# Kernel optimization log

Measured on AMD Instinct MI355X. Metric: run time of the kernel, lower is better.

Reference implementation:

```python
import jax, jax.numpy as jnp
import numpy as np

CUTOFF = 2.0
LOG2 = float(np.log(2.0))

def ssp(x):
    # shifted softplus: softplus(x) - log(2)
    return jax.nn.softplus(x) - LOG2

def setup_inputs() -> dict:
    key = jax.random.key(0)
    ks = jax.random.split(key, 12)
    N, E, H, F, G = 10000, 320000, 256, 256, 50
    x = jax.random.normal(ks[0], (N, H), dtype=jnp.float32)
    edge_index = jax.random.randint(ks[1], (2, E), 0, N, dtype=jnp.int64)
    edge_weight = jax.random.normal(ks[2], (E, 3), dtype=jnp.float32)
    edge_attr = jax.random.normal(ks[3], (E, G), dtype=jnp.float32)
    s = lambda fan_in: 1.0 / np.sqrt(fan_in)
    mlp_w1 = jax.random.uniform(ks[4], (G, F), jnp.float32, -s(G), s(G))
    mlp_b1 = jax.random.uniform(ks[5], (F,), jnp.float32, -s(G), s(G))
    mlp_w2 = jax.random.uniform(ks[6], (F, F), jnp.float32, -s(F), s(F))
    mlp_b2 = jax.random.uniform(ks[7], (F,), jnp.float32, -s(F), s(F))
    lin1_w = jax.random.uniform(ks[8], (H, F), jnp.float32, -s(H), s(H))
    lin2_w = jax.random.uniform(ks[9], (F, H), jnp.float32, -s(F), s(F))
    lin2_b = jax.random.uniform(ks[10], (H,), jnp.float32, -s(F), s(F))
    return {"x": x, "edge_index": edge_index, "edge_weight": edge_weight,
            "edge_attr": edge_attr, "mlp_w1": mlp_w1, "mlp_b1": mlp_b1,
            "mlp_w2": mlp_w2, "mlp_b2": mlp_b2, "lin1_w": lin1_w,
            "lin2_w": lin2_w, "lin2_b": lin2_b}

def reference(x, edge_index, edge_weight, edge_attr,
              mlp_w1, mlp_b1, mlp_w2, mlp_b2, lin1_w, lin2_w, lin2_b):
    N = x.shape[0]
    # cutoff envelope on edge distances
    distances = jnp.linalg.norm(edge_weight, axis=1)                 # [E]
    C = 0.5 * (jnp.cos(distances * jnp.pi / CUTOFF) + 1.0)
    C = C * (distances <= CUTOFF)                                    # [E]
    # edge filter MLP
    W = ssp(edge_attr @ mlp_w1 + mlp_b1) @ mlp_w2 + mlp_b2           # [E, F]
    W = W * C[:, None]
    i, j = edge_index[0], edge_index[1]
    messages = W * (x[j] @ lin1_w)                                   # [E, F]
    agg = jax.ops.segment_sum(messages, i, num_segments=N)           # [N, F]
    h = ssp(agg @ lin2_w + lin2_b)                                   # [N, H]
    return x + h
```

## Files before the change

### kernel.cpp

```cpp
#include <hip/hip_runtime.h>
#include <hip/hip_bf16.h>
#include <stdint.h>

#define HF 256
#define GG 50

typedef __attribute__((ext_vector_type(8))) short bf16x8;
typedef __attribute__((ext_vector_type(4))) short bf16x4;
typedef __attribute__((ext_vector_type(4))) float f32x4;

__device__ __forceinline__ uint32_t f2bf2u(float a, float b){
    __hip_bfloat162 h = __float22bfloat162_rn(make_float2(a, b));
    union { __hip_bfloat162 h; uint32_t u; } v; v.h = h; return v.u;
}
__device__ __forceinline__ short f2bf(float x){
    union { float f; uint32_t u; } v; v.f = x;
    uint32_t r = (v.u + 0x7FFFu + ((v.u >> 16) & 1u)) >> 16;
    return (short)(uint16_t)r;
}
__device__ __forceinline__ float bf2f(short s){
    union { uint32_t u; float f; } v; v.u = ((uint32_t)(uint16_t)s) << 16;
    return v.f;
}
__device__ __forceinline__ float ssp_f(float x){
    return fmaxf(x, 0.f) + __logf(1.f + __expf(-fabsf(x))) - 0.69314718055994531f;
}

__device__ __forceinline__ void pack_natural(const float* __restrict__ B,
                                             short* __restrict__ Bp,
                                             int idx, int KT, int kmax)
{
    int lane = idx & 63;
    int kt   = (idx >> 6) & (KT - 1);
    int ntg  = idx >> (6 + (KT == 2 ? 1 : 3));
    int col  = ntg * 16 + (lane & 15);
    int k0   = kt * 32 + (lane >> 4) * 8;
    uint32_t u[4];
#pragma unroll
    for (int jj = 0; jj < 4; ++jj) {
        int ka = k0 + 2*jj, kb = k0 + 2*jj + 1;
        float a = (ka < kmax) ? B[(size_t)ka * HF + col] : 0.f;
        float b = (kb < kmax) ? B[(size_t)kb * HF + col] : 0.f;
        u[jj] = f2bf2u(a, b);
    }
    *(uint4*)&Bp[(size_t)idx * 8] = *(uint4*)u;
}

__global__ __launch_bounds__(256)
void prep_kernel(const float* __restrict__ w1, const float* __restrict__ w2,
                 const float* __restrict__ lin1, const float* __restrict__ lin2,
                 short* __restrict__ w1p, short* __restrict__ w2p,
                 short* __restrict__ lin1p, short* __restrict__ lin2p,
                 const float* __restrict__ x, short* __restrict__ x_bf, int nx8,
                 const int* __restrict__ eidx, int* __restrict__ cnt, int E, int gConv)
{
    int b = blockIdx.x, tid = threadIdx.x;
    if (b < 8) {
        pack_natural(w1, w1p, b * 256 + tid, 2, GG);
    } else if (b < 40) {
        int idx = (b - 8) * 256 + tid;
        int lane = idx & 63;
        int kt   = (idx >> 6) & 7;
        int ntg  = idx >> 9;
        int col  = ntg * 16 + (lane & 15);
        int s0   = kt * 32 + (lane >> 4) * 8;
        uint32_t u[4];
#pragma unroll
        for (int jj = 0; jj < 4; ++jj) {
            int sa = s0 + 2*jj, sb = sa + 1;
            int fa = (sa >> 6) * 64 + (sa & 3) * 16 + ((sa & 63) >> 2);
            int fb = (sb >> 6) * 64 + (sb & 3) * 16 + ((sb & 63) >> 2);
            u[jj] = f2bf2u(w2[(size_t)fa * HF + col], w2[(size_t)fb * HF + col]);
        }
        *(uint4*)&w2p[(size_t)idx * 8] = *(uint4*)u;
    } else if (b < 72) {
        pack_natural(lin1, lin1p, (b - 40) * 256 + tid, 8, HF);
    } else if (b < 104) {
        pack_natural(lin2, lin2p, (b - 72) * 256 + tid, 8, HF);
    } else if (b < 104 + gConv) {
        int idx = (b - 104) * 256 + tid;
        if (idx < nx8) {
            const float* xp = x + (size_t)idx * 8;
            float4 p0 = *(const float4*)(xp);
            float4 p1 = *(const float4*)(xp + 4);
            uint32_t u[4] = { f2bf2u(p0.x, p0.y), f2bf2u(p0.z, p0.w),
                              f2bf2u(p1.x, p1.y), f2bf2u(p1.z, p1.w) };
            *(uint4*)&x_bf[(size_t)idx * 8] = *(uint4*)u;
        }
    } else {
        int e = (b - 104 - gConv) * 256 + tid;
        if (e < E) atomicAdd(&cnt[eidx[e]], 1);
    }
}

__global__ __launch_bounds__(256)
void scan_kernel(const int* __restrict__ cnt, int* __restrict__ row,
                 int* __restrict__ cursor, int N, int E)
{
    __shared__ int part[256];
    const int t = threadIdx.x;
    const int CH = (N + 255) / 256;
    int lo = t * CH;
    int hi = min(lo + CH, N);
    int s = 0;
    for (int n = lo; n < hi; ++n) s += cnt[n];
    part[t] = s;
    __syncthreads();
    for (int off = 1; off < 256; off <<= 1) {
        int v = (t >= off) ? part[t - off] : 0;
        __syncthreads();
        part[t] += v;
        __syncthreads();
    }
    int acc = part[t] - s;
    for (int n = lo; n < hi; ++n) {
        row[n] = acc; cursor[n] = acc;
        acc += cnt[n];
    }
    if (t == 255) row[N] = E;
}

__global__ __launch_bounds__(256)
void mid_kernel(const int* __restrict__ eidx, int* __restrict__ cursor,
                int* __restrict__ perm, int E, int gScatter,
                const short* __restrict__ x_bf, const short* __restrict__ lin1p,
                short* __restrict__ y_p, int N)
{
    const int tid = threadIdx.x;
    if ((int)blockIdx.x < gScatter) {
        int e = blockIdx.x * 256 + tid;
        if (e < E) {
            int pos = atomicAdd(&cursor[eidx[e]], 1);
            perm[pos] = e;
        }
        return;
    }
    const int blk  = blockIdx.x - gScatter;
    const int lane = tid & 63;
    const int w    = tid >> 6;
    const int l15  = lane & 15;
    const int quad = lane >> 4;
    const int row0 = blk * 64;

    f32x4 acc[4][4];
#pragma unroll
    for (int mt = 0; mt < 4; ++mt)
#pragma unroll
        for (int nt = 0; nt < 4; ++nt)
            acc[mt][nt] = (f32x4){0.f, 0.f, 0.f, 0.f};

#pragma unroll 2
    for (int kt = 0; kt < 8; ++kt) {
        bf16x8 af[4];
#pragma unroll
        for (int mt = 0; mt < 4; ++mt) {
            int r = row0 + mt * 16 + l15;
            int rl = (r < N) ? r : 0;
            af[mt] = *(const bf16x8*)&x_bf[(size_t)rl * HF + kt * 32 + quad * 8];
        }
#pragma unroll
        for (int nt = 0; nt < 4; ++nt) {
            bf16x8 bfr = *(const bf16x8*)&lin1p[(size_t)(((w * 4 + nt) * 8 + kt) * 64 + lane) * 8];
#pragma unroll
            for (int mt = 0; mt < 4; ++mt)
                acc[mt][nt] = __builtin_amdgcn_mfma_f32_16x16x32_bf16(af[mt], bfr, acc[mt][nt], 0, 0, 0);
        }
    }
#pragma unroll
    for (int mt = 0; mt < 4; ++mt) {
#pragma unroll
        for (int r = 0; r < 4; ++r) {
            int row = row0 + mt * 16 + quad * 4 + r;
            if (row < N) {
                uint2 u = make_uint2(f2bf2u(acc[mt][0][r], acc[mt][1][r]),
                                     f2bf2u(acc[mt][2][r], acc[mt][3][r]));
                *(uint2*)&y_p[(size_t)row * HF + w * 64 + l15 * 4] = u;
            }
        }
    }
}

__global__ __launch_bounds__(256)
void node2_kernel(const float* __restrict__ agg, const short* __restrict__ lin2p,
                  const float* __restrict__ bias, const float* __restrict__ x,
                  float* __restrict__ out, int N)
{
    const int tid  = threadIdx.x;
    const int lane = tid & 63;
    const int w    = tid >> 6;
    const int l15  = lane & 15;
    const int quad = lane >> 4;
    const int row0 = blockIdx.x * 64;

    f32x4 acc[4][4];
#pragma unroll
    for (int mt = 0; mt < 4; ++mt)
#pragma unroll
        for (int nt = 0; nt < 4; ++nt)
            acc[mt][nt] = (f32x4){0.f, 0.f, 0.f, 0.f};

#pragma unroll 2
    for (int kt = 0; kt < 8; ++kt) {
        bf16x8 af[4];
#pragma unroll
        for (int mt = 0; mt < 4; ++mt) {
            int r = row0 + mt * 16 + l15;
            int rl = (r < N) ? r : 0;
            const float* ap = agg + (size_t)rl * HF + kt * 32 + quad * 8;
            float4 p0 = *(const float4*)(ap);
            float4 p1 = *(const float4*)(ap + 4);
            union { uint32_t u[4]; bf16x8 v; } c;
            c.u[0] = f2bf2u(p0.x, p0.y); c.u[1] = f2bf2u(p0.z, p0.w);
            c.u[2] = f2bf2u(p1.x, p1.y); c.u[3] = f2bf2u(p1.z, p1.w);
            af[mt] = c.v;
        }
#pragma unroll
        for (int nt = 0; nt < 4; ++nt) {
            bf16x8 bfr = *(const bf16x8*)&lin2p[(size_t)(((w * 4 + nt) * 8 + kt) * 64 + lane) * 8];
#pragma unroll
            for (int mt = 0; mt < 4; ++mt)
                acc[mt][nt] = __builtin_amdgcn_mfma_f32_16x16x32_bf16(af[mt], bfr, acc[mt][nt], 0, 0, 0);
        }
    }
    float bs[4];
#pragma unroll
    for (int nt = 0; nt < 4; ++nt) bs[nt] = bias[w * 64 + nt * 16 + l15];
#pragma unroll
    for (int mt = 0; mt < 4; ++mt) {
#pragma unroll
        for (int r = 0; r < 4; ++r) {
            int row = row0 + mt * 16 + quad * 4 + r;
            if (row < N) {
#pragma unroll
                for (int nt = 0; nt < 4; ++nt) {
                    int f = w * 64 + nt * 16 + l15;
                    float v = ssp_f(acc[mt][nt][r] + bs[nt]) + x[(size_t)row * HF + f];
                    out[(size_t)row * HF + f] = v;
                }
            }
        }
    }
}

__global__ __launch_bounds__(256, 3)
void edge_mfma(const float* __restrict__ ea, const int* __restrict__ eidx,
               const float* __restrict__ ew,
               const short* __restrict__ w1p, const float* __restrict__ b1,
               const short* __restrict__ w2p, const float* __restrict__ b2,
               const short* __restrict__ y_p, const int* __restrict__ perm,
               const int* __restrict__ rowp,
               float* __restrict__ agg, int E)
{
    __shared__ short smem[21504];
    short* ea_b = smem;
    short* hid  = smem + 4608;
    short* msgT = smem;
    __shared__ int s_e[64], s_i[64], s_j[64];
    __shared__ float s_c[64];
    __shared__ unsigned long long s_bmask;

    const int tid  = threadIdx.x;
    const int lane = tid & 63;
    const int w    = tid >> 6;
    const int l15  = lane & 15;
    const int quad = lane >> 4;
    const int e0   = blockIdx.x * 64;

    if (tid < 64) {
        int p = e0 + tid;
        int e = 0, iv = -1, jv = 0;
        float c = 0.f;
        if (p < E) {
            e  = perm[p];
            iv = eidx[e];
            jv = eidx[E + e];
            float d0 = ew[e*3+0], d1 = ew[e*3+1], d2 = ew[e*3+2];
            float d = sqrtf(d0*d0 + d1*d1 + d2*d2);
            c = (d <= 2.0f) ? 0.5f * (__cosf(d * 1.57079632679489662f) + 1.0f) : 0.f;
        }
        s_e[tid] = e; s_i[tid] = iv; s_j[tid] = jv; s_c[tid] = c;
        int ivn = __shfl_down(iv, 1);
        bool flag = (tid == 63) || (iv != ivn);
        unsigned long long m = __ballot(flag);
        if (tid == 0) s_bmask = m;
    }
    __syncthreads();

    for (int idx = tid; idx < 64 * 25; idx += 256) {
        int e = idx / 25, p = idx - e * 25;
        const float* sp = ea + (size_t)s_e[e] * GG + p * 2;
        float2 v = *(const float2*)sp;
        *(uint32_t*)&ea_b[e * 72 + p * 2] = f2bf2u(v.x, v.y);
    }
    for (int idx = tid; idx < 64 * 7; idx += 256) {
        int e = idx / 7, q = idx - e * 7;
        *(uint32_t*)&ea_b[e * 72 + 50 + q * 2] = 0u;
    }
    __syncthreads();

    f32x4 acc1[4][4];
#pragma unroll
    for (int mt = 0; mt < 4; ++mt)
#pragma unroll
        for (int nt = 0; nt < 4; ++nt)
            acc1[mt][nt] = (f32x4){0.f, 0.f, 0.f, 0.f};

#pragma unroll
    for (int kt = 0; kt < 2; ++kt) {
        bf16x8 af[4];
#pragma unroll
        for (int mt = 0; mt < 4; ++mt)
            af[mt] = *(bf16x8*)&ea_b[(mt * 16 + l15) * 72 + kt * 32 + quad * 8];
#pragma unroll
        for (int nt = 0; nt < 4; ++nt) {
            bf16x8 bfr = *(const bf16x8*)&w1p[(size_t)(((w * 4 + nt) * 2 + kt) * 64 + lane) * 8];
#pragma unroll
            for (int mt = 0; mt < 4; ++mt)
                acc1[mt][nt] = __builtin_amdgcn_mfma_f32_16x16x32_bf16(af[mt], bfr, acc1[mt][nt], 0, 0, 0);
        }
    }

    float bias1[4];
#pragma unroll
    for (int nt = 0; nt < 4; ++nt) bias1[nt] = b1[w * 64 + nt * 16 + l15];
#pragma unroll
    for (int mt = 0; mt < 4; ++mt) {
#pragma unroll
        for (int r = 0; r < 4; ++r) {
            int e = mt * 16 + quad * 4 + r;
            float v0 = ssp_f(acc1[mt][0][r] + bias1[0]);
            float v1 = ssp_f(acc1[mt][1][r] + bias1[1]);
            float v2 = ssp_f(acc1[mt][2][r] + bias1[2]);
            float v3 = ssp_f(acc1[mt][3][r] + bias1[3]);
            uint2 u = make_uint2(f2bf2u(v0, v1), f2bf2u(v2, v3));
            *(uint2*)&hid[e * 264 + w * 64 + l15 * 4] = u;
        }
    }
    __syncthreads();

    bf16x4 yv[4][4];
#pragma unroll
    for (int mt = 0; mt < 4; ++mt)
#pragma unroll
        for (int r = 0; r < 4; ++r) {
            int e = mt * 16 + quad * 4 + r;
            yv[mt][r] = *(const bf16x4*)&y_p[(size_t)s_j[e] * HF + w * 64 + l15 * 4];
        }

    f32x4 acc2[4][4];
#pragma unroll
    for (int mt = 0; mt < 4; ++mt)
#pragma unroll
        for (int nt = 0; nt < 4; ++nt)
            acc2[mt][nt] = (f32x4){0.f, 0.f, 0.f, 0.f};

#pragma unroll 2
    for (int kt = 0; kt < 8; ++kt) {
        bf16x8 af[4];
#pragma unroll
        for (int mt = 0; mt < 4; ++mt)
            af[mt] = *(bf16x8*)&hid[(mt * 16 + l15) * 264 + kt * 32 + quad * 8];
#pragma unroll
        for (int nt = 0; nt < 4; ++nt) {
            bf16x8 bfr = *(const bf16x8*)&w2p[(size_t)(((w * 4 + nt) * 8 + kt) * 64 + lane) * 8];
#pragma unroll
            for (int mt = 0; mt < 4; ++mt)
                acc2[mt][nt] = __builtin_amdgcn_mfma_f32_16x16x32_bf16(af[mt], bfr, acc2[mt][nt], 0, 0, 0);
        }
    }
    __syncthreads();

    float bias2[4];
#pragma unroll
    for (int nt = 0; nt < 4; ++nt) bias2[nt] = b2[w * 64 + nt * 16 + l15];
    float cs[4][4];
#pragma unroll
    for (int mt = 0; mt < 4; ++mt)
#pragma unroll
        for (int r = 0; r < 4; ++r)
            cs[mt][r] = s_c[mt * 16 + quad * 4 + r];
#pragma unroll
    for (int mt = 0; mt < 4; ++mt) {
#pragma unroll
        for (int nt = 0; nt < 4; ++nt) {
            int col = w * 64 + nt * 16 + l15;
            float v0 = (acc2[mt][nt][0] + bias2[nt]) * cs[mt][0] * bf2f(yv[mt][0][nt]);
            float v1 = (acc2[mt][nt][1] + bias2[nt]) * cs[mt][1] * bf2f(yv[mt][1][nt]);
            float v2 = (acc2[mt][nt][2] + bias2[nt]) * cs[mt][2] * bf2f(yv[mt][2][nt]);
            float v3 = (acc2[mt][nt][3] + bias2[nt]) * cs[mt][3] * bf2f(yv[mt][3][nt]);
            uint2 u = make_uint2(f2bf2u(v0, v1), f2bf2u(v2, v3));
            *(uint2*)&msgT[col * 68 + mt * 16 + quad * 4] = u;
        }
    }
    __syncthreads();

    {
        unsigned long long bm = s_bmask;
        unsigned mlo = __builtin_amdgcn_readfirstlane((unsigned)bm);
        unsigned mhi = __builtin_amdgcn_readfirstlane((unsigned)(bm >> 32));
        const int col = tid;
        float sum = 0.f;
#pragma unroll
        for (int ch = 0; ch < 8; ++ch) {
            bf16x8 v = *(bf16x8*)&msgT[col * 68 + ch * 8];
#pragma unroll
            for (int j = 0; j < 8; ++j) {
                int e = ch * 8 + j;
                sum += bf2f(v[j]);
                unsigned bit = (e < 32) ? ((mlo >> e) & 1u) : ((mhi >> (e - 32)) & 1u);
                if (bit) {
                    int node = __builtin_amdgcn_readfirstlane(s_i[e]);
                    if (node >= 0) {
                        int lo = rowp[node], hi = rowp[node + 1];
                        float* ap = agg + (size_t)node * HF + col;
                        if (lo >= e0 && hi <= e0 + 64) *ap = sum;
                        else atomicAdd(ap, sum);
                    }
                    sum = 0.f;
                }
            }
        }
    }
}

extern "C" void kernel_launch(void* const* d_in, const int* in_sizes, int n_in,
                              void* d_out, int out_size, void* d_ws, size_t ws_size,
                              hipStream_t stream)
{
    const float* x     = (const float*)d_in[0];
    const int*   eidx  = (const int*)  d_in[1];
    const float* ew    = (const float*)d_in[2];
    const float* ea    = (const float*)d_in[3];
    const float* w1    = (const float*)d_in[4];
    const float* b1    = (const float*)d_in[5];
    const float* w2    = (const float*)d_in[6];
    const float* b2    = (const float*)d_in[7];
    const float* lin1  = (const float*)d_in[8];
    const float* lin2  = (const float*)d_in[9];
    const float* lin2b = (const float*)d_in[10];
    float* out = (float*)d_out;

    const int N = in_sizes[0] / HF;
    const int E = in_sizes[2] / 3;

    const size_t fN = (size_t)N * HF;
    float* agg    = (float*)d_ws;
    short* y_p    = (short*)(agg + fN);
    short* x_bf   = y_p + fN;
    int*   cnt    = (int*)(x_bf + fN);
    int*   row    = cnt + N;
    int*   cursor = row + (N + 8);
    int*   perm   = cursor + N;
    short* w1p    = (short*)(((uintptr_t)(perm + E) + 255) & ~(uintptr_t)255);
    short* w2p    = w1p + 16384;
    short* lin1p  = w2p + 65536;
    short* lin2p  = lin1p + 65536;

    hipMemsetAsync(cnt, 0, (size_t)N * sizeof(int), stream);
    hipMemsetAsync(agg, 0, fN * sizeof(float), stream);

    const int nx8   = (int)(fN / 8);
    const int gConv = (nx8 + 255) / 256;
    const int gHist = (E + 255) / 256;
    prep_kernel<<<dim3(104 + gConv + gHist), dim3(256), 0, stream>>>(
        w1, w2, lin1, lin2, w1p, w2p, lin1p, lin2p, x, x_bf, nx8, eidx, cnt, E, gConv);

    scan_kernel<<<dim3(1), dim3(256), 0, stream>>>(cnt, row, cursor, N, E);

    const int gScatter = (E + 255) / 256;
    const int gNode    = (N + 63) / 64;
    mid_kernel<<<dim3(gScatter + gNode), dim3(256), 0, stream>>>(
        eidx, cursor, perm, E, gScatter, x_bf, lin1p, y_p, N);

    edge_mfma<<<dim3((E + 63) / 64), dim3(256), 0, stream>>>(
        ea, eidx, ew, w1p, b1, w2p, b2, y_p, perm, row, agg, E);

    node2_kernel<<<dim3(gNode), dim3(256), 0, stream>>>(
        agg, lin2p, lin2b, x, out, N);
}
```

Measured before the change: 346.6 us.

## Fuse all stages into one persistent cooperative kernel with grid syncs

```diff
diff --git a/kernel.cpp b/kernel.cpp
--- a/kernel.cpp
+++ b/kernel.cpp
@@ -1,6 +1,9 @@
 #include <hip/hip_runtime.h>
 #include <hip/hip_bf16.h>
+#include <hip/hip_cooperative_groups.h>
 #include <stdint.h>
+
+namespace cg = cooperative_groups;
 
 #define HF 256
 #define GG 50
@@ -13,11 +16,6 @@
     __hip_bfloat162 h = __float22bfloat162_rn(make_float2(a, b));
     union { __hip_bfloat162 h; uint32_t u; } v; v.h = h; return v.u;
 }
-__device__ __forceinline__ short f2bf(float x){
-    union { float f; uint32_t u; } v; v.f = x;
-    uint32_t r = (v.u + 0x7FFFu + ((v.u >> 16) & 1u)) >> 16;
-    return (short)(uint16_t)r;
-}
 __device__ __forceinline__ float bf2f(short s){
     union { uint32_t u; float f; } v; v.u = ((uint32_t)(uint16_t)s) << 16;
     return v.f;
@@ -26,19 +24,37 @@
     return fmaxf(x, 0.f) + __logf(1.f + __expf(-fabsf(x))) - 0.69314718055994531f;
 }
 
-__device__ __forceinline__ void pack_natural(const float* __restrict__ B,
-                                             short* __restrict__ Bp,
-                                             int idx, int KT, int kmax)
+struct Params {
+    const float *x; const int *eidx; const float *ew; const float *ea;
+    const float *w1, *b1, *w2, *b2, *lin1, *lin2, *lin2b;
+    float *out;
+    float *agg; short *y_p, *x_bf;
+    int *cnt, *row, *cursor, *perm, *partial;
+    short *w1p, *w2p, *lin1p, *lin2p;
+    int N, E, nTiles, eTiles;
+};
+
+struct EdgeSmem {
+    short smem[21504];
+    int s_e[64], s_i[64], s_j[64];
+    float s_c[64];
+    unsigned long long bmask;
+    int scanbuf[256];
+};
+
+__device__ __forceinline__ void pack_nat(const float* __restrict__ B,
+                                         short* __restrict__ Bp,
+                                         int idx, int ktBits, int kmax)
 {
     int lane = idx & 63;
-    int kt   = (idx >> 6) & (KT - 1);
-    int ntg  = idx >> (6 + (KT == 2 ? 1 : 3));
+    int kt   = (idx >> 6) & ((1 << ktBits) - 1);
+    int ntg  = idx >> (6 + ktBits);
     int col  = ntg * 16 + (lane & 15);
     int k0   = kt * 32 + (lane >> 4) * 8;
     uint32_t u[4];
 #pragma unroll
     for (int jj = 0; jj < 4; ++jj) {
-        int ka = k0 + 2*jj, kb = k0 + 2*jj + 1;
+        int ka = k0 + 2*jj, kb = ka + 1;
         float a = (ka < kmax) ? B[(size_t)ka * HF + col] : 0.f;
         float b = (kb < kmax) ? B[(size_t)kb * HF + col] : 0.f;
         u[jj] = f2bf2u(a, b);
@@ -46,108 +62,57 @@
     *(uint4*)&Bp[(size_t)idx * 8] = *(uint4*)u;
 }
 
-__global__ __launch_bounds__(256)
-void prep_kernel(const float* __restrict__ w1, const float* __restrict__ w2,
-                 const float* __restrict__ lin1, const float* __restrict__ lin2,
-                 short* __restrict__ w1p, short* __restrict__ w2p,
-                 short* __restrict__ lin1p, short* __restrict__ lin2p,
-                 const float* __restrict__ x, short* __restrict__ x_bf, int nx8,
-                 const int* __restrict__ eidx, int* __restrict__ cnt, int E, int gConv)
-{
-    int b = blockIdx.x, tid = threadIdx.x;
-    if (b < 8) {
-        pack_natural(w1, w1p, b * 256 + tid, 2, GG);
-    } else if (b < 40) {
-        int idx = (b - 8) * 256 + tid;
-        int lane = idx & 63;
-        int kt   = (idx >> 6) & 7;
-        int ntg  = idx >> 9;
-        int col  = ntg * 16 + (lane & 15);
-        int s0   = kt * 32 + (lane >> 4) * 8;
-        uint32_t u[4];
-#pragma unroll
-        for (int jj = 0; jj < 4; ++jj) {
-            int sa = s0 + 2*jj, sb = sa + 1;
-            int fa = (sa >> 6) * 64 + (sa & 3) * 16 + ((sa & 63) >> 2);
-            int fb = (sb >> 6) * 64 + (sb & 3) * 16 + ((sb & 63) >> 2);
-            u[jj] = f2bf2u(w2[(size_t)fa * HF + col], w2[(size_t)fb * HF + col]);
-        }
-        *(uint4*)&w2p[(size_t)idx * 8] = *(uint4*)u;
-    } else if (b < 72) {
-        pack_natural(lin1, lin1p, (b - 40) * 256 + tid, 8, HF);
-    } else if (b < 104) {
-        pack_natural(lin2, lin2p, (b - 72) * 256 + tid, 8, HF);
-    } else if (b < 104 + gConv) {
-        int idx = (b - 104) * 256 + tid;
-        if (idx < nx8) {
-            const float* xp = x + (size_t)idx * 8;
-            float4 p0 = *(const float4*)(xp);
-            float4 p1 = *(const float4*)(xp + 4);
-            uint32_t u[4] = { f2bf2u(p0.x, p0.y), f2bf2u(p0.z, p0.w),
-                              f2bf2u(p1.x, p1.y), f2bf2u(p1.z, p1.w) };
-            *(uint4*)&x_bf[(size_t)idx * 8] = *(uint4*)u;
-        }
-    } else {
-        int e = (b - 104 - gConv) * 256 + tid;
-        if (e < E) atomicAdd(&cnt[eidx[e]], 1);
-    }
-}
-
-__global__ __launch_bounds__(256)
-void scan_kernel(const int* __restrict__ cnt, int* __restrict__ row,
-                 int* __restrict__ cursor, int N, int E)
-{
-    __shared__ int part[256];
-    const int t = threadIdx.x;
-    const int CH = (N + 255) / 256;
-    int lo = t * CH;
-    int hi = min(lo + CH, N);
-    int s = 0;
-    for (int n = lo; n < hi; ++n) s += cnt[n];
-    part[t] = s;
-    __syncthreads();
-    for (int off = 1; off < 256; off <<= 1) {
-        int v = (t >= off) ? part[t - off] : 0;
-        __syncthreads();
-        part[t] += v;
-        __syncthreads();
-    }
-    int acc = part[t] - s;
-    for (int n = lo; n < hi; ++n) {
-        row[n] = acc; cursor[n] = acc;
-        acc += cnt[n];
-    }
-    if (t == 255) row[N] = E;
-}
-
-__global__ __launch_bounds__(256)
-void mid_kernel(const int* __restrict__ eidx, int* __restrict__ cursor,
-                int* __restrict__ perm, int E, int gScatter,
-                const short* __restrict__ x_bf, const short* __restrict__ lin1p,
-                short* __restrict__ y_p, int N)
-{
-    const int tid = threadIdx.x;
-    if ((int)blockIdx.x < gScatter) {
-        int e = blockIdx.x * 256 + tid;
-        if (e < E) {
-            int pos = atomicAdd(&cursor[eidx[e]], 1);
-            perm[pos] = e;
-        }
-        return;
-    }
-    const int blk  = blockIdx.x - gScatter;
-    const int lane = tid & 63;
-    const int w    = tid >> 6;
-    const int l15  = lane & 15;
-    const int quad = lane >> 4;
-    const int row0 = blk * 64;
+__device__ __forceinline__ void pack_w2i(const float* __restrict__ w2,
+                                         short* __restrict__ w2p, int idx)
+{
+    int lane = idx & 63;
+    int kt   = (idx >> 6) & 7;
+    int ntg  = idx >> 9;
+    int col  = ntg * 16 + (lane & 15);
+    int s0   = kt * 32 + (lane >> 4) * 8;
+    uint32_t u[4];
+#pragma unroll
+    for (int jj = 0; jj < 4; ++jj) {
+        int sa = s0 + 2*jj, sb = sa + 1;
+        int fa = (sa >> 6) * 64 + (sa & 3) * 16 + ((sa & 63) >> 2);
+        int fb = (sb >> 6) * 64 + (sb & 3) * 16 + ((sb & 63) >> 2);
+        u[jj] = f2bf2u(w2[(size_t)fa * HF + col], w2[(size_t)fb * HF + col]);
+    }
+    *(uint4*)&w2p[(size_t)idx * 8] = *(uint4*)u;
+}
+
+__device__ __forceinline__ void phaseA(const Params& p, int gtid, int gstr)
+{
+    for (int i = gtid; i < p.N; i += gstr) p.cnt[i] = 0;
+    float4 z = make_float4(0.f, 0.f, 0.f, 0.f);
+    int nAgg4 = p.N * (HF / 4);
+    for (int i = gtid; i < nAgg4; i += gstr) ((float4*)p.agg)[i] = z;
+    for (int i = gtid; i < 2048; i += gstr) pack_nat(p.w1, p.w1p, i, 1, GG);
+    for (int i = gtid; i < 8192; i += gstr) pack_w2i(p.w2, p.w2p, i);
+    for (int i = gtid; i < 8192; i += gstr) pack_nat(p.lin1, p.lin1p, i, 3, HF);
+    for (int i = gtid; i < 8192; i += gstr) pack_nat(p.lin2, p.lin2p, i, 3, HF);
+    int nx8 = p.N * (HF / 8);
+    for (int i = gtid; i < nx8; i += gstr) {
+        const float* xp = p.x + (size_t)i * 8;
+        float4 p0 = *(const float4*)(xp);
+        float4 p1 = *(const float4*)(xp + 4);
+        uint32_t u[4] = { f2bf2u(p0.x, p0.y), f2bf2u(p0.z, p0.w),
+                          f2bf2u(p1.x, p1.y), f2bf2u(p1.z, p1.w) };
+        *(uint4*)&p.x_bf[(size_t)i * 8] = *(uint4*)u;
+    }
+}
+
+__device__ __forceinline__ void node1_tile(const Params& p, int t)
+{
+    const int tid  = threadIdx.x;
+    const int lane = tid & 63, w = tid >> 6, l15 = lane & 15, quad = lane >> 4;
+    const int row0 = t * 64;
 
     f32x4 acc[4][4];
 #pragma unroll
     for (int mt = 0; mt < 4; ++mt)
 #pragma unroll
-        for (int nt = 0; nt < 4; ++nt)
-            acc[mt][nt] = (f32x4){0.f, 0.f, 0.f, 0.f};
+        for (int nt = 0; nt < 4; ++nt) acc[mt][nt] = (f32x4){0.f,0.f,0.f,0.f};
 
 #pragma unroll 2
     for (int kt = 0; kt < 8; ++kt) {
@@ -155,12 +120,12 @@
 #pragma unroll
         for (int mt = 0; mt < 4; ++mt) {
             int r = row0 + mt * 16 + l15;
-            int rl = (r < N) ? r : 0;
-            af[mt] = *(const bf16x8*)&x_bf[(size_t)rl * HF + kt * 32 + quad * 8];
+            int rl = (r < p.N) ? r : 0;
+            af[mt] = *(const bf16x8*)&p.x_bf[(size_t)rl * HF + kt * 32 + quad * 8];
         }
 #pragma unroll
         for (int nt = 0; nt < 4; ++nt) {
-            bf16x8 bfr = *(const bf16x8*)&lin1p[(size_t)(((w * 4 + nt) * 8 + kt) * 64 + lane) * 8];
+            bf16x8 bfr = *(const bf16x8*)&p.lin1p[(size_t)(((w*4+nt)*8+kt)*64+lane)*8];
 #pragma unroll
             for (int mt = 0; mt < 4; ++mt)
                 acc[mt][nt] = __builtin_amdgcn_mfma_f32_16x16x32_bf16(af[mt], bfr, acc[mt][nt], 0, 0, 0);
@@ -171,33 +136,26 @@
 #pragma unroll
         for (int r = 0; r < 4; ++r) {
             int row = row0 + mt * 16 + quad * 4 + r;
-            if (row < N) {
+            if (row < p.N) {
                 uint2 u = make_uint2(f2bf2u(acc[mt][0][r], acc[mt][1][r]),
                                      f2bf2u(acc[mt][2][r], acc[mt][3][r]));
-                *(uint2*)&y_p[(size_t)row * HF + w * 64 + l15 * 4] = u;
+                *(uint2*)&p.y_p[(size_t)row * HF + w * 64 + l15 * 4] = u;
             }
         }
     }
 }
 
-__global__ __launch_bounds__(256)
-void node2_kernel(const float* __restrict__ agg, const short* __restrict__ lin2p,
-                  const float* __restrict__ bias, const float* __restrict__ x,
-                  float* __restrict__ out, int N)
+__device__ __forceinline__ void node2_tile(const Params& p, int t)
 {
     const int tid  = threadIdx.x;
-    const int lane = tid & 63;
-    const int w    = tid >> 6;
-    const int l15  = lane & 15;
-    const int quad = lane >> 4;
-    const int row0 = blockIdx.x * 64;
+    const int lane = tid & 63, w = tid >> 6, l15 = lane & 15, quad = lane >> 4;
+    const int row0 = t * 64;
 
     f32x4 acc[4][4];
 #pragma unroll
     for (int mt = 0; mt < 4; ++mt)
 #pragma unroll
-        for (int nt = 0; nt < 4; ++nt)
-            acc[mt][nt] = (f32x4){0.f, 0.f, 0.f, 0.f};
+        for (int nt = 0; nt < 4; ++nt) acc[mt][nt] = (f32x4){0.f,0.f,0.f,0.f};
 
 #pragma unroll 2
     for (int kt = 0; kt < 8; ++kt) {
@@ -205,8 +163,8 @@
 #pragma unroll
         for (int mt = 0; mt < 4; ++mt) {
             int r = row0 + mt * 16 + l15;
-            int rl = (r < N) ? r : 0;
-            const float* ap = agg + (size_t)rl * HF + kt * 32 + quad * 8;
+            int rl = (r < p.N) ? r : 0;
+            const float* ap = p.agg + (size_t)rl * HF + kt * 32 + quad * 8;
             float4 p0 = *(const float4*)(ap);
             float4 p1 = *(const float4*)(ap + 4);
             union { uint32_t u[4]; bf16x8 v; } c;
@@ -216,7 +174,7 @@
         }
 #pragma unroll
         for (int nt = 0; nt < 4; ++nt) {
-            bf16x8 bfr = *(const bf16x8*)&lin2p[(size_t)(((w * 4 + nt) * 8 + kt) * 64 + lane) * 8];
+            bf16x8 bfr = *(const bf16x8*)&p.lin2p[(size_t)(((w*4+nt)*8+kt)*64+lane)*8];
 #pragma unroll
             for (int mt = 0; mt < 4; ++mt)
                 acc[mt][nt] = __builtin_amdgcn_mfma_f32_16x16x32_bf16(af[mt], bfr, acc[mt][nt], 0, 0, 0);
@@ -224,75 +182,63 @@
     }
     float bs[4];
 #pragma unroll
-    for (int nt = 0; nt < 4; ++nt) bs[nt] = bias[w * 64 + nt * 16 + l15];
+    for (int nt = 0; nt < 4; ++nt) bs[nt] = p.lin2b[w * 64 + nt * 16 + l15];
 #pragma unroll
     for (int mt = 0; mt < 4; ++mt) {
 #pragma unroll
         for (int r = 0; r < 4; ++r) {
             int row = row0 + mt * 16 + quad * 4 + r;
-            if (row < N) {
+            if (row < p.N) {
 #pragma unroll
                 for (int nt = 0; nt < 4; ++nt) {
                     int f = w * 64 + nt * 16 + l15;
-                    float v = ssp_f(acc[mt][nt][r] + bs[nt]) + x[(size_t)row * HF + f];
-                    out[(size_t)row * HF + f] = v;
+                    float v = ssp_f(acc[mt][nt][r] + bs[nt]) + p.x[(size_t)row * HF + f];
+                    p.out[(size_t)row * HF + f] = v;
                 }
             }
         }
     }
 }
 
-__global__ __launch_bounds__(256, 3)
-void edge_mfma(const float* __restrict__ ea, const int* __restrict__ eidx,
-               const float* __restrict__ ew,
-               const short* __restrict__ w1p, const float* __restrict__ b1,
-               const short* __restrict__ w2p, const float* __restrict__ b2,
-               const short* __restrict__ y_p, const int* __restrict__ perm,
-               const int* __restrict__ rowp,
-               float* __restrict__ agg, int E)
-{
-    __shared__ short smem[21504];
-    short* ea_b = smem;
-    short* hid  = smem + 4608;
-    short* msgT = smem;
-    __shared__ int s_e[64], s_i[64], s_j[64];
-    __shared__ float s_c[64];
-    __shared__ unsigned long long s_bmask;
-
+__device__ __forceinline__ void edge_tile(EdgeSmem& S, const Params& p, int t,
+    const bf16x8 (&w1f)[2][4], const float (&bias1)[4], const float (&bias2)[4])
+{
+    short* ea_b = S.smem;
+    short* hid  = S.smem + 4608;
+    short* msgT = S.smem;
     const int tid  = threadIdx.x;
-    const int lane = tid & 63;
-    const int w    = tid >> 6;
-    const int l15  = lane & 15;
-    const int quad = lane >> 4;
-    const int e0   = blockIdx.x * 64;
+    const int lane = tid & 63, w = tid >> 6, l15 = lane & 15, quad = lane >> 4;
+    const int e0   = t * 64;
+
+    __syncthreads();
 
     if (tid < 64) {
-        int p = e0 + tid;
+        int pp = e0 + tid;
         int e = 0, iv = -1, jv = 0;
         float c = 0.f;
-        if (p < E) {
-            e  = perm[p];
-            iv = eidx[e];
-            jv = eidx[E + e];
-            float d0 = ew[e*3+0], d1 = ew[e*3+1], d2 = ew[e*3+2];
+        if (pp < p.E) {
+            e  = p.perm[pp];
+            iv = p.eidx[e];
+            jv = p.eidx[p.E + e];
+            float d0 = p.ew[e*3+0], d1 = p.ew[e*3+1], d2 = p.ew[e*3+2];
             float d = sqrtf(d0*d0 + d1*d1 + d2*d2);
             c = (d <= 2.0f) ? 0.5f * (__cosf(d * 1.57079632679489662f) + 1.0f) : 0.f;
         }
-        s_e[tid] = e; s_i[tid] = iv; s_j[tid] = jv; s_c[tid] = c;
+        S.s_e[tid] = e; S.s_i[tid] = iv; S.s_j[tid] = jv; S.s_c[tid] = c;
         int ivn = __shfl_down(iv, 1);
         bool flag = (tid == 63) || (iv != ivn);
         unsigned long long m = __ballot(flag);
-        if (tid == 0) s_bmask = m;
-    }
-    __syncthreads();
-
-    for (int idx = tid; idx < 64 * 25; idx += 256) {
-        int e = idx / 25, p = idx - e * 25;
-        const float* sp = ea + (size_t)s_e[e] * GG + p * 2;
+        if (tid == 0) S.bmask = m;
+    }
+    __syncthreads();
+
+    for (int idx = tid; idx < 1600; idx += 256) {
+        int e = idx / 25, q = idx - e * 25;
+        const float* sp = p.ea + (size_t)S.s_e[e] * GG + q * 2;
         float2 v = *(const float2*)sp;
-        *(uint32_t*)&ea_b[e * 72 + p * 2] = f2bf2u(v.x, v.y);
-    }
-    for (int idx = tid; idx < 64 * 7; idx += 256) {
+        *(uint32_t*)&ea_b[e * 72 + q * 2] = f2bf2u(v.x, v.y);
+    }
+    for (int idx = tid; idx < 448; idx += 256) {
         int e = idx / 7, q = idx - e * 7;
         *(uint32_t*)&ea_b[e * 72 + 50 + q * 2] = 0u;
     }
@@ -302,8 +248,7 @@
 #pragma unroll
     for (int mt = 0; mt < 4; ++mt)
 #pragma unroll
-        for (int nt = 0; nt < 4; ++nt)
-            acc1[mt][nt] = (f32x4){0.f, 0.f, 0.f, 0.f};
+        for (int nt = 0; nt < 4; ++nt) acc1[mt][nt] = (f32x4){0.f,0.f,0.f,0.f};
 
 #pragma unroll
     for (int kt = 0; kt < 2; ++kt) {
@@ -312,17 +257,12 @@
         for (int mt = 0; mt < 4; ++mt)
             af[mt] = *(bf16x8*)&ea_b[(mt * 16 + l15) * 72 + kt * 32 + quad * 8];
 #pragma unroll
-        for (int nt = 0; nt < 4; ++nt) {
-            bf16x8 bfr = *(const bf16x8*)&w1p[(size_t)(((w * 4 + nt) * 2 + kt) * 64 + lane) * 8];
+        for (int nt = 0; nt < 4; ++nt)
 #pragma unroll
             for (int mt = 0; mt < 4; ++mt)
-                acc1[mt][nt] = __builtin_amdgcn_mfma_f32_16x16x32_bf16(af[mt], bfr, acc1[mt][nt], 0, 0, 0);
-        }
-    }
-
-    float bias1[4];
-#pragma unroll
-    for (int nt = 0; nt < 4; ++nt) bias1[nt] = b1[w * 64 + nt * 16 + l15];
+                acc1[mt][nt] = __builtin_amdgcn_mfma_f32_16x16x32_bf16(af[mt], w1f[kt][nt], acc1[mt][nt], 0, 0, 0);
+    }
+
 #pragma unroll
     for (int mt = 0; mt < 4; ++mt) {
 #pragma unroll
@@ -344,15 +284,14 @@
 #pragma unroll
         for (int r = 0; r < 4; ++r) {
             int e = mt * 16 + quad * 4 + r;
-            yv[mt][r] = *(const bf16x4*)&y_p[(size_t)s_j[e] * HF + w * 64 + l15 * 4];
+            yv[mt][r] = *(const bf16x4*)&p.y_p[(size_t)S.s_j[e] * HF + w * 64 + l15 * 4];
         }
 
     f32x4 acc2[4][4];
 #pragma unroll
     for (int mt = 0; mt < 4; ++mt)
 #pragma unroll
-        for (int nt = 0; nt < 4; ++nt)
-            acc2[mt][nt] = (f32x4){0.f, 0.f, 0.f, 0.f};
+        for (int nt = 0; nt < 4; ++nt) acc2[mt][nt] = (f32x4){0.f,0.f,0.f,0.f};
 
 #pragma unroll 2
     for (int kt = 0; kt < 8; ++kt) {
@@ -362,7 +301,7 @@
             af[mt] = *(bf16x8*)&hid[(mt * 16 + l15) * 264 + kt * 32 + quad * 8];
 #pragma unroll
         for (int nt = 0; nt < 4; ++nt) {
-            bf16x8 bfr = *(const bf16x8*)&w2p[(size_t)(((w * 4 + nt) * 8 + kt) * 64 + lane) * 8];
+            bf16x8 bfr = *(const bf16x8*)&p.w2p[(size_t)(((w*4+nt)*8+kt)*64+lane)*8];
 #pragma unroll
             for (int mt = 0; mt < 4; ++mt)
                 acc2[mt][nt] = __builtin_amdgcn_mfma_f32_16x16x32_bf16(af[mt], bfr, acc2[mt][nt], 0, 0, 0);
@@ -370,15 +309,12 @@
     }
     __syncthreads();
 
-    float bias2[4];
-#pragma unroll
-    for (int nt = 0; nt < 4; ++nt) bias2[nt] = b2[w * 64 + nt * 16 + l15];
     float cs[4][4];
 #pragma unroll
     for (int mt = 0; mt < 4; ++mt)
 #pragma unroll
         for (int r = 0; r < 4; ++r)
-            cs[mt][r] = s_c[mt * 16 + quad * 4 + r];
+            cs[mt][r] = S.s_c[mt * 16 + quad * 4 + r];
 #pragma unroll
     for (int mt = 0; mt < 4; ++mt) {
 #pragma unroll
@@ -395,7 +331,7 @@
     __syncthreads();
 
     {
-        unsigned long long bm = s_bmask;
+        unsigned long long bm = S.bmask;
         unsigned mlo = __builtin_amdgcn_readfirstlane((unsigned)bm);
         unsigned mhi = __builtin_amdgcn_readfirstlane((unsigned)(bm >> 32));
         const int col = tid;
@@ -409,10 +345,10 @@
                 sum += bf2f(v[j]);
                 unsigned bit = (e < 32) ? ((mlo >> e) & 1u) : ((mhi >> (e - 32)) & 1u);
                 if (bit) {
-                    int node = __builtin_amdgcn_readfirstlane(s_i[e]);
+                    int node = __builtin_amdgcn_readfirstlane(S.s_i[e]);
                     if (node >= 0) {
-                        int lo = rowp[node], hi = rowp[node + 1];
-                        float* ap = agg + (size_t)node * HF + col;
+                        int lo = p.row[node], hi = p.row[node + 1];
+                        float* ap = p.agg + (size_t)node * HF + col;
                         if (lo >= e0 && hi <= e0 + 64) *ap = sum;
                         else atomicAdd(ap, sum);
                     }
@@ -423,58 +359,238 @@
     }
 }
 
+__device__ __forceinline__ void edge_phase(EdgeSmem& S, const Params& p, int stride)
+{
+    const int tid  = threadIdx.x;
+    const int lane = tid & 63, w = tid >> 6, l15 = lane & 15;
+    bf16x8 w1f[2][4];
+#pragma unroll
+    for (int kt = 0; kt < 2; ++kt)
+#pragma unroll
+        for (int nt = 0; nt < 4; ++nt)
+            w1f[kt][nt] = *(const bf16x8*)&p.w1p[(size_t)(((w*4+nt)*2+kt)*64+lane)*8];
+    float bias1[4], bias2[4];
+#pragma unroll
+    for (int nt = 0; nt < 4; ++nt) {
+        bias1[nt] = p.b1[w * 64 + nt * 16 + l15];
+        bias2[nt] = p.b2[w * 64 + nt * 16 + l15];
+    }
+    for (int t = blockIdx.x; t < p.eTiles; t += stride)
+        edge_tile(S, p, t, w1f, bias1, bias2);
+}
+
+__global__ __launch_bounds__(256, 3)
+void mega(Params p)
+{
+    cg::grid_group grid = cg::this_grid();
+    __shared__ EdgeSmem S;
+    const int G    = gridDim.x;
+    const int tid  = threadIdx.x;
+    const int gtid = blockIdx.x * 256 + tid;
+    const int gstr = G * 256;
+
+    phaseA(p, gtid, gstr);
+    grid.sync();
+
+    for (int e = gtid; e < p.E; e += gstr) atomicAdd(&p.cnt[p.eidx[e]], 1);
+    for (int t = blockIdx.x; t < p.nTiles; t += G) node1_tile(p, t);
+    grid.sync();
+
+    const int CH = (p.N + G - 1) / G;
+    const int lo = blockIdx.x * CH;
+    const int hi = min(lo + CH, p.N);
+    {
+        int s = 0;
+        for (int n = lo + tid; n < hi; n += 256) s += p.cnt[n];
+        S.scanbuf[tid] = s;
+        __syncthreads();
+#pragma unroll
+        for (int off = 128; off > 0; off >>= 1) {
+            if (tid < off) S.scanbuf[tid] += S.scanbuf[tid + off];
+            __syncthreads();
+        }
+        if (tid == 0) p.partial[blockIdx.x] = S.scanbuf[0];
+    }
+    grid.sync();
+
+    if (blockIdx.x == 0) {
+        int b4 = tid * 4;
+        int a[4]; int ls = 0;
+#pragma unroll
+        for (int q = 0; q < 4; ++q) { a[q] = (b4 + q < G) ? p.partial[b4 + q] : 0; ls += a[q]; }
+        S.scanbuf[tid] = ls;
+        __syncthreads();
+        for (int off = 1; off < 256; off <<= 1) {
+            int v = (tid >= off) ? S.scanbuf[tid - off] : 0;
+            __syncthreads();
+            S.scanbuf[tid] += v;
+            __syncthreads();
+        }
+        int ex = S.scanbuf[tid] - ls;
+#pragma unroll
+        for (int q = 0; q < 4; ++q) { if (b4 + q < G) p.partial[b4 + q] = ex; ex += a[q]; }
+    }
+    grid.sync();
+
+    {
+        int c = 0;
+        if (lo + tid < hi) c = p.cnt[lo + tid];
+        S.scanbuf[tid] = c;
+        __syncthreads();
+        if (tid == 0) {
+            int acc = p.partial[blockIdx.x];
+            int m = hi - lo;
+            for (int k = 0; k < m; ++k) {
+                p.row[lo + k] = acc; p.cursor[lo + k] = acc;
+                acc += S.scanbuf[k];
+            }
+        }
+        if (gtid == 0) p.row[p.N] = p.E;
+    }
+    grid.sync();
+
+    for (int e = gtid; e < p.E; e += gstr) {
+        int pos = atomicAdd(&p.cursor[p.eidx[e]], 1);
+        p.perm[pos] = e;
+    }
+    grid.sync();
+
+    edge_phase(S, p, G);
+    grid.sync();
+
+    for (int t = blockIdx.x; t < p.nTiles; t += G) node2_tile(p, t);
+}
+
+__global__ __launch_bounds__(256)
+void fb_prep(Params p)
+{
+    const int gtid = blockIdx.x * 256 + threadIdx.x;
+    const int gstr = gridDim.x * 256;
+    for (int i = gtid; i < 2048; i += gstr) pack_nat(p.w1, p.w1p, i, 1, GG);
+    for (int i = gtid; i < 8192; i += gstr) pack_w2i(p.w2, p.w2p, i);
+    for (int i = gtid; i < 8192; i += gstr) pack_nat(p.lin1, p.lin1p, i, 3, HF);
+    for (int i = gtid; i < 8192; i += gstr) pack_nat(p.lin2, p.lin2p, i, 3, HF);
+    int nx8 = p.N * (HF / 8);
+    for (int i = gtid; i < nx8; i += gstr) {
+        const float* xp = p.x + (size_t)i * 8;
+        float4 p0 = *(const float4*)(xp);
+        float4 p1 = *(const float4*)(xp + 4);
+        uint32_t u[4] = { f2bf2u(p0.x, p0.y), f2bf2u(p0.z, p0.w),
+                          f2bf2u(p1.x, p1.y), f2bf2u(p1.z, p1.w) };
+        *(uint4*)&p.x_bf[(size_t)i * 8] = *(uint4*)u;
+    }
+    for (int e = gtid; e < p.E; e += gstr) atomicAdd(&p.cnt[p.eidx[e]], 1);
+}
+
+__global__ __launch_bounds__(256)
+void fb_scan(Params p)
+{
+    __shared__ int part[256];
+    const int t = threadIdx.x;
+    const int CH = (p.N + 255) / 256;
+    int lo = t * CH, hi = min(lo + CH, p.N);
+    int s = 0;
+    for (int n = lo; n < hi; ++n) s += p.cnt[n];
+    part[t] = s;
+    __syncthreads();
+    for (int off = 1; off < 256; off <<= 1) {
+        int v = (t >= off) ? part[t - off] : 0;
+        __syncthreads();
+        part[t] += v;
+        __syncthreads();
+    }
+    int acc = part[t] - s;
+    for (int n = lo; n < hi; ++n) {
+        p.row[n] = acc; p.cursor[n] = acc;
+        acc += p.cnt[n];
+    }
+    if (t == 255) p.row[p.N] = p.E;
+}
+
+__global__ __launch_bounds__(256)
+void fb_mid(Params p)
+{
+    const int gtid = blockIdx.x * 256 + threadIdx.x;
+    const int gstr = gridDim.x * 256;
+    for (int e = gtid; e < p.E; e += gstr) {
+        int pos = atomicAdd(&p.cursor[p.eidx[e]], 1);
+        p.perm[pos] = e;
+    }
+    for (int t = blockIdx.x; t < p.nTiles; t += gridDim.x) node1_tile(p, t);
+}
+
+__global__ __launch_bounds__(256, 3)
+void fb_edge(Params p)
+{
+    __shared__ EdgeSmem S;
+    edge_phase(S, p, gridDim.x);
+}
+
+__global__ __launch_bounds__(256)
+void fb_node2(Params p)
+{
+    for (int t = blockIdx.x; t < p.nTiles; t += gridDim.x) node2_tile(p, t);
+}
+
 extern "C" void kernel_launch(void* const* d_in, const int* in_sizes, int n_in,
                               void* d_out, int out_size, void* d_ws, size_t ws_size,
                               hipStream_t stream)
 {
-    const float* x     = (const float*)d_in[0];
-    const int*   eidx  = (const int*)  d_in[1];
-    const float* ew    = (const float*)d_in[2];
-    const float* ea    = (const float*)d_in[3];
-    const float* w1    = (const float*)d_in[4];
-    const float* b1    = (const float*)d_in[5];
-    const float* w2    = (const float*)d_in[6];
-    const float* b2    = (const float*)d_in[7];
-    const float* lin1  = (const float*)d_in[8];
-    const float* lin2  = (const float*)d_in[9];
-    const float* lin2b = (const float*)d_in[10];
-    float* out = (float*)d_out;
+    Params p;
+    p.x    = (const float*)d_in[0];
+    p.eidx = (const int*)  d_in[1];
+    p.ew   = (const float*)d_in[2];
+    p.ea   = (const float*)d_in[3];
+    p.w1   = (const float*)d_in[4];
+    p.b1   = (const float*)d_in[5];
+    p.w2   = (const float*)d_in[6];
+    p.b2   = (const float*)d_in[7];
+    p.lin1 = (const float*)d_in[8];
+    p.lin2 = (const float*)d_in[9];
+    p.lin2b= (const float*)d_in[10];
+    p.out  = (float*)d_out;
 
     const int N = in_sizes[0] / HF;
     const int E = in_sizes[2] / 3;
+    p.N = N; p.E = E;
+    p.nTiles = (N + 63) / 64;
+    p.eTiles = (E + 63) / 64;
 
     const size_t fN = (size_t)N * HF;
-    float* agg    = (float*)d_ws;
-    short* y_p    = (short*)(agg + fN);
-    short* x_bf   = y_p + fN;
-    int*   cnt    = (int*)(x_bf + fN);
-    int*   row    = cnt + N;
-    int*   cursor = row + (N + 8);
-    int*   perm   = cursor + N;
-    short* w1p    = (short*)(((uintptr_t)(perm + E) + 255) & ~(uintptr_t)255);
-    short* w2p    = w1p + 16384;
-    short* lin1p  = w2p + 65536;
-    short* lin2p  = lin1p + 65536;
-
-    hipMemsetAsync(cnt, 0, (size_t)N * sizeof(int), stream);
-    hipMemsetAsync(agg, 0, fN * sizeof(float), stream);
-
-    const int nx8   = (int)(fN / 8);
-    const int gConv = (nx8 + 255) / 256;
-    const int gHist = (E + 255) / 256;
-    prep_kernel<<<dim3(104 + gConv + gHist), dim3(256), 0, stream>>>(
-        w1, w2, lin1, lin2, w1p, w2p, lin1p, lin2p, x, x_bf, nx8, eidx, cnt, E, gConv);
-
-    scan_kernel<<<dim3(1), dim3(256), 0, stream>>>(cnt, row, cursor, N, E);
-
-    const int gScatter = (E + 255) / 256;
-    const int gNode    = (N + 63) / 64;
-    mid_kernel<<<dim3(gScatter + gNode), dim3(256), 0, stream>>>(
-        eidx, cursor, perm, E, gScatter, x_bf, lin1p, y_p, N);
-
-    edge_mfma<<<dim3((E + 63) / 64), dim3(256), 0, stream>>>(
-        ea, eidx, ew, w1p, b1, w2p, b2, y_p, perm, row, agg, E);
-
-    node2_kernel<<<dim3(gNode), dim3(256), 0, stream>>>(
-        agg, lin2p, lin2b, x, out, N);
-}
+    p.agg     = (float*)d_ws;
+    p.y_p     = (short*)(p.agg + fN);
+    p.x_bf    = p.y_p + fN;
+    p.cnt     = (int*)(p.x_bf + fN);
+    p.row     = p.cnt + N;
+    p.cursor  = p.row + (N + 8);
+    p.perm    = p.cursor + N;
+    p.partial = p.perm + E;
+    p.w1p     = (short*)(((uintptr_t)(p.partial + 1040) + 255) & ~(uintptr_t)255);
+    p.w2p     = p.w1p + 16384;
+    p.lin1p   = p.w2p + 65536;
+    p.lin2p   = p.lin1p + 65536;
+
+    int dev = 0; hipGetDevice(&dev);
+    int nCU = 0;
+    hipDeviceGetAttribute(&nCU, hipDeviceAttributeMultiprocessorCount, dev);
+    int maxb = 0;
+    hipError_t oe = hipOccupancyMaxActiveBlocksPerMultiprocessor(&maxb, mega, 256, 0);
+    int G = (oe == hipSuccess && maxb > 0 && nCU > 0) ? maxb * nCU : 0;
+    if (G > 1024) G = 1024;
+
+    bool done = false;
+    if (G >= 64) {
+        void* args[] = { (void*)&p };
+        done = (hipLaunchCooperativeKernel(mega, dim3(G), dim3(256), args, 0, stream)
+                == hipSuccess);
+    }
+    if (!done) {
+        hipMemsetAsync(p.cnt, 0, (size_t)N * sizeof(int), stream);
+        hipMemsetAsync(p.agg, 0, fN * sizeof(float), stream);
+        fb_prep <<<dim3(1024), dim3(256), 0, stream>>>(p);
+        fb_scan <<<dim3(1),    dim3(256), 0, stream>>>(p);
+        fb_mid  <<<dim3(1024), dim3(256), 0, stream>>>(p);
+        fb_edge <<<dim3(p.eTiles), dim3(256), 0, stream>>>(p);
+        fb_node2<<<dim3(p.nTiles), dim3(256), 0, stream>>>(p);
+    }
+}
```

New measurement: 807.9 us. +133.1%, slower.
